# Kernel optimization log

Hardware: AMD Instinct MI355X
Metric: run time of the kernel (lower is better)

## Reference

```python
import jax, jax.numpy as jnp
import numpy as np

# --- static configuration (from init_kwargs / chosen original_size) ---
IMG = 1024            # PromptGetter image_size
DS = 64               # PromptGetter downsizing
ORIG_H, ORIG_W = 1080, 1920
SCALE = IMG / max(ORIG_H, ORIG_W)                 # ResizeLongestSide scale
PRE_H = int(np.floor(ORIG_H * SCALE + 0.5))       # get_prepadded_size -> 576
PRE_W = int(np.floor(ORIG_W * SCALE + 0.5))       # -> 1024
NW = int(ORIG_W * SCALE) // DS                    # grid columns (n_w)
NUM_GRIDS = (IMG // DS) ** 2                      # safe upper bound on grid ids (256)
DEFAULT_THR_TARGET = 0.65
NUM_BG = 1
NUM_LABELS = 16


def setup_inputs() -> dict:
    key = jax.random.key(0)
    k1, k2 = jax.random.split(key)
    return {
        "image_embeddings": jax.random.normal(k1, (1, 256, 64, 64), dtype=jnp.float32),
        "reference_feats": jax.random.normal(k2, (NUM_LABELS, 1, 256), dtype=jnp.float32),
        "original_size": jnp.array([ORIG_H, ORIG_W], dtype=jnp.int32),
        "threshold": jnp.zeros((1, 1), dtype=jnp.float32),  # 0 -> default_threshold_target
        "num_bg_points": 1,
    }


def _postprocess(sim):
    """SAM postprocess_masks: 64x64 -> IMGxIMG -> crop prepadded -> original size."""
    m = jax.image.resize(sim, (IMG, IMG), method="linear")  # align_corners=False bilinear
    m = m[:PRE_H, :PRE_W]
    return jax.image.resize(m, (ORIG_H, ORIG_W), method="linear")


def _point_selection(mask_sim, thr):
    h, w = mask_sim.shape
    flat = mask_sim.reshape(-1)

    # background: k lowest-similarity points (topk largest=False)
    _, bg_idx = jax.lax.top_k(-flat, NUM_BG)
    bg_row = bg_idx // w
    bg_col = bg_idx - bg_row * w
    bg_coords = jnp.stack([bg_col, bg_row], axis=-1).astype(jnp.float32)  # (NUM_BG, 2) as (x, y)

    # foreground: per-grid-cell best-scoring point above threshold.
    # The original gathers torch.where(mask_sim > thr) points and picks the max
    # score per downsized grid cell; here we keep fixed shapes by masking and
    # doing a segment-max over all pixels (same selected points/scores).
    idx = jnp.arange(h * w)
    ys = idx // w
    xs = idx % w
    valid = flat > thr
    grid = ((jnp.floor(ys * SCALE / DS)) * NW + jnp.floor(xs * SCALE / DS)).astype(jnp.int32)
    score = jnp.where(valid, flat, -jnp.inf)
    best = jax.ops.segment_max(score, grid, num_segments=NUM_GRIDS)
    is_best = valid & (flat == best[grid])
    cand = jnp.where(is_best, idx, h * w)
    best_idx = jax.ops.segment_min(cand, grid, num_segments=NUM_GRIDS)  # first max, like torch.topk(k=1)
    grid_ok = jnp.isfinite(best) & (best_idx < h * w)
    safe_idx = jnp.minimum(best_idx, h * w - 1)
    bx = jnp.where(grid_ok, (safe_idx % w).astype(jnp.float32), 0.0)
    by = jnp.where(grid_ok, (safe_idx // w).astype(jnp.float32), 0.0)
    sc = jnp.where(grid_ok, best, -jnp.inf)
    pts = jnp.stack([bx, by, sc], axis=-1)  # (NUM_GRIDS, 3) = (x, y, score)

    # sort by score, descending (empty grid cells sink to the end with -inf)
    order = jnp.argsort(-pts[:, -1])
    return pts[order], bg_coords


def reference(image_embeddings, reference_feats, original_size, threshold, num_bg_points):
    tf = image_embeddings[0]                                   # (C, H, W)
    tf = tf / jnp.linalg.norm(tf, axis=0, keepdims=True)       # channelwise L2 normalize
    c = tf.shape[0]
    tf = tf.reshape(c, -1)                                     # (C, HW)
    thr = ((threshold == 0).astype(threshold.dtype) * DEFAULT_THR_TARGET + threshold)[0, 0]

    def per_label(ref_feat):                                   # ref_feat (1, C)
        sim = (ref_feat @ tf).reshape(64, 64)                  # cosine sim map
        return _point_selection(_postprocess(sim), thr)

    points_scores, bg_coords = jax.vmap(per_label)(reference_feats)
    return points_scores, bg_coords
```

## Files before the change

kernel.cpp:

```cpp
#include <hip/hip_runtime.h>
#include <cmath>
#include <climits>

#define NLAB 16
#define GRIDS 144
#define HOUT 1080
#define WOUT 1920
#define KS2 0.53333336f
#define KS1 0.0625f
#define NEG_MARK -1.0e30f
#define POS_BIG   1.0e30f

__device__ __forceinline__ void taps64(int i, int& t0, int& t1, float& g) {
    float s = ((float)i + 0.5f) * KS1 - 0.5f;
    float f = floorf(s);
    g = s - f;
    int j = (int)f;
    t0 = j < 0 ? 0 : j;
    t1 = j + 1; if (t1 > 63) t1 = 63;
}

__device__ __forceinline__ void fused_taps(int P, int n1m1, int& base,
                                           float& w0, float& w1, float& w2) {
    float sx = ((float)P + 0.5f) * KS2 - 0.5f;
    float fx = floorf(sx);
    float bx = sx - fx;
    int tx = (int)fx;
    int i0 = tx < 0 ? 0 : tx;
    int i1 = tx + 1; if (i1 > n1m1) i1 = n1m1;
    int a0, a1; float ga; taps64(i0, a0, a1, ga);
    int b0, b1; float gb; taps64(i1, b0, b1, gb);
    base = a0;
    w0 = (1.f - bx) * (1.f - ga); w1 = 0.f; w2 = 0.f;
    float c1 = (1.f - bx) * ga;
    if (a1 == base) w0 += c1; else w1 += c1;
    float c2 = bx * (1.f - gb);
    { int o = b0 - base; if (o == 0) w0 += c2; else if (o == 1) w1 += c2; else w2 += c2; }
    float c3 = bx * gb;
    { int o = b1 - base; if (o == 0) w0 += c3; else if (o == 1) w1 += c3; else w2 += c3; }
}

__launch_bounds__(256)
__global__ void sim_kernel(const float* __restrict__ emb,
                           const float* __restrict__ ref,
                           float* __restrict__ sim) {
    __shared__ float rlds[NLAB * 256];
    __shared__ float red[16][NLAB][16];
    __shared__ float n2red[16][16];
    int tid = threadIdx.x;
    for (int i = tid; i < NLAB * 256; i += 256) rlds[i] = ref[i];
    __syncthreads();
    int posl = tid & 15;
    int chunk = tid >> 4;
    int p = blockIdx.x * 16 + posl;
    float acc[NLAB];
#pragma unroll
    for (int l = 0; l < NLAB; ++l) acc[l] = 0.f;
    float n2 = 0.f;
    int cbase = chunk * 16;
#pragma unroll
    for (int cc = 0; cc < 16; ++cc) {
        int c = cbase + cc;
        float v = emb[c * 4096 + p];
        n2 = fmaf(v, v, n2);
#pragma unroll
        for (int l = 0; l < NLAB; ++l)
            acc[l] = fmaf(rlds[l * 256 + c], v, acc[l]);
    }
#pragma unroll
    for (int l = 0; l < NLAB; ++l) red[posl][l][chunk] = acc[l];
    n2red[posl][chunk] = n2;
    __syncthreads();
    int l = chunk;
    float dot = 0.f, nn = 0.f;
#pragma unroll
    for (int k = 0; k < 16; ++k) { dot += red[posl][l][k]; nn += n2red[posl][k]; }
    sim[l * 4096 + p] = dot / sqrtf(nn);
}

__launch_bounds__(256)
__global__ void eval_kernel(const float* __restrict__ simAll,
                            const float* __restrict__ thrPtr,
                            float* __restrict__ gVal, int* __restrict__ gIdx,
                            float* __restrict__ mVal, int* __restrict__ mIdx) {
    int label = blockIdx.x / GRIDS;
    int g = blockIdx.x - label * GRIDS;
    int gy = g >> 4, gx = g & 15;
    int tid = threadIdx.x;

    __shared__ float s8[8][9];
    __shared__ float4 wxT[120];
    __shared__ float4 wyT[120];
    __shared__ float rv[4], rmv[4];
    __shared__ int   ri[4], rmi[4];

    int X0 = gx * 120, Y0 = gy * 120;
    int r0, c0; float dw0, dw1, dw2;
    fused_taps(Y0, 575, r0, dw0, dw1, dw2);
    fused_taps(X0, 1023, c0, dw0, dw1, dw2);

    if (tid < 64) {
        int j = tid >> 3, k = tid & 7;
        int rr = r0 + j; if (rr > 63) rr = 63;
        int kk = c0 + k; if (kk > 63) kk = 63;
        s8[j][k] = simAll[label * 4096 + rr * 64 + kk];
    }
    if (tid < 120) {
        int kb; float w0, w1, w2;
        fused_taps(X0 + tid, 1023, kb, w0, w1, w2);
        wxT[tid] = make_float4(w0, w1, w2, __int_as_float(kb - c0));
    } else if (tid >= 128 && tid < 248) {
        int r = tid - 128;
        int rb; float w0, w1, w2;
        fused_taps(Y0 + r, 575, rb, w0, w1, w2);
        wyT[r] = make_float4(w0, w1, w2, __int_as_float(rb - r0));
    }
    __syncthreads();

    float t0v = thrPtr[0];
    float thr = (t0v == 0.0f) ? 0.65f : t0v;

    float bmax = NEG_MARK; int bidx = INT_MAX;
    float vmin = POS_BIG;  int vidx = INT_MAX;

    if (tid < 240) {
        int h = (tid >= 120) ? 1 : 0;
        int c = tid - h * 120;
        float4 wx = wxT[c];
        int kb = __float_as_int(wx.w);
        const int ybase = h * 60;
        int idx = (Y0 + ybase) * WOUT + X0 + c;
        int rcur = -1;
        float t0 = 0.f, t1 = 0.f, t2 = 0.f;
#pragma unroll 4
        for (int r = 0; r < 60; ++r) {
            float4 wy = wyT[ybase + r];
            int rb = __float_as_int(wy.w);
            if (rb != rcur) {
                rcur = rb;
                const float* p0 = &s8[rb][kb];
                const float* p1 = &s8[rb + 1][kb];
                const float* p2 = &s8[rb + 2][kb];
                t0 = fmaf(wx.z, p0[2], fmaf(wx.y, p0[1], wx.x * p0[0]));
                t1 = fmaf(wx.z, p1[2], fmaf(wx.y, p1[1], wx.x * p1[0]));
                t2 = fmaf(wx.z, p2[2], fmaf(wx.y, p2[1], wx.x * p2[0]));
            }
            float val = fmaf(wy.z, t2, fmaf(wy.y, t1, wy.x * t0));
            if (val > bmax) { bmax = val; bidx = idx; }
            if (val < vmin) { vmin = val; vidx = idx; }
            idx += WOUT;
        }
    }

    for (int off = 32; off; off >>= 1) {
        float ov = __shfl_xor(bmax, off); int oi = __shfl_xor(bidx, off);
        if (ov > bmax || (ov == bmax && oi < bidx)) { bmax = ov; bidx = oi; }
        float mv2 = __shfl_xor(vmin, off); int mi2 = __shfl_xor(vidx, off);
        if (mv2 < vmin || (mv2 == vmin && mi2 < vidx)) { vmin = mv2; vidx = mi2; }
    }
    int wave = tid >> 6;
    if ((tid & 63) == 0) { rv[wave] = bmax; ri[wave] = bidx; rmv[wave] = vmin; rmi[wave] = vidx; }
    __syncthreads();
    if (tid == 0) {
#pragma unroll
        for (int w = 1; w < 4; ++w) {
            float ov = rv[w]; int oi = ri[w];
            if (ov > rv[0] || (ov == rv[0] && oi < ri[0])) { rv[0] = ov; ri[0] = oi; }
            float mv2 = rmv[w]; int mi2 = rmi[w];
            if (mv2 < rmv[0] || (mv2 == rmv[0] && mi2 < rmi[0])) { rmv[0] = mv2; rmi[0] = mi2; }
        }
        int o = label * GRIDS + g;
        if (rv[0] > thr) { gVal[o] = rv[0]; gIdx[o] = ri[0]; }
        else             { gVal[o] = NEG_MARK; gIdx[o] = INT_MAX; }
        mVal[o] = rmv[0]; mIdx[o] = rmi[0];
    }
}

__launch_bounds__(256)
__global__ void final_kernel(const float* __restrict__ gVal, const int* __restrict__ gIdx,
                             const float* __restrict__ mVal, const int* __restrict__ mIdx,
                             float* __restrict__ out) {
    int l = blockIdx.x;
    int tid = threadIdx.x;
    __shared__ float sc[256]; __shared__ int sg[256];
    __shared__ float lx[256], ly[256];

    float score = NEG_MARK;
    float x = 0.0f, y = 0.0f;
    if (tid < GRIDS) {
        float v = gVal[l * GRIDS + tid];
        int i = gIdx[l * GRIDS + tid];
        if (v != NEG_MARK && i < HOUT * WOUT) {
            score = v;
            x = (float)(i % WOUT);
            y = (float)(i / WOUT);
        }
    }
    sc[tid] = score; sg[tid] = tid; lx[tid] = x; ly[tid] = y;
    __syncthreads();

    for (int k = 2; k <= 256; k <<= 1) {
        for (int j = k >> 1; j > 0; j >>= 1) {
            int i2 = tid ^ j;
            if (i2 > tid) {
                float s_a = sc[tid], s_b = sc[i2];
                int g_a = sg[tid], g_b = sg[i2];
                bool up = ((tid & k) == 0);
                bool b_before_a = (s_b > s_a) || (s_b == s_a && g_b < g_a);
                if (b_before_a == up) {
                    sc[tid] = s_b; sc[i2] = s_a;
                    sg[tid] = g_b; sg[i2] = g_a;
                }
            }
            __syncthreads();
        }
    }

    int g2 = sg[tid];
    float* o = out + (l * 256 + tid) * 3;
    o[0] = lx[g2]; o[1] = ly[g2]; o[2] = sc[tid];

    __shared__ float mv[256]; __shared__ int mi[256];
    float v2 = POS_BIG; int i3 = INT_MAX;
    if (tid < GRIDS) { v2 = mVal[l * GRIDS + tid]; i3 = mIdx[l * GRIDS + tid]; }
    mv[tid] = v2; mi[tid] = i3;
    __syncthreads();
    for (int s2 = 128; s2 > 0; s2 >>= 1) {
        if (tid < s2) {
            float ov = mv[tid + s2]; int oi = mi[tid + s2];
            if (ov < mv[tid] || (ov == mv[tid] && oi < mi[tid])) { mv[tid] = ov; mi[tid] = oi; }
        }
        __syncthreads();
    }
    if (tid == 0) {
        int bi = mi[0];
        out[NLAB * 256 * 3 + l * 2 + 0] = (float)(bi % WOUT);
        out[NLAB * 256 * 3 + l * 2 + 1] = (float)(bi / WOUT);
    }
}

extern "C" void kernel_launch(void* const* d_in, const int* in_sizes, int n_in,
                              void* d_out, int out_size, void* d_ws, size_t ws_size,
                              hipStream_t stream) {
    const float* emb = (const float*)d_in[0];
    const float* ref = (const float*)d_in[1];
    const float* thr = (const float*)d_in[3];
    float* out = (float*)d_out;

    float* sim  = (float*)d_ws;
    float* gVal = sim + NLAB * 4096;
    int*   gIdx = (int*)(gVal + NLAB * GRIDS);
    float* mVal = (float*)(gIdx + NLAB * GRIDS);
    int*   mIdx = (int*)(mVal + NLAB * GRIDS);

    sim_kernel<<<256, 256, 0, stream>>>(emb, ref, sim);
    eval_kernel<<<NLAB * GRIDS, 256, 0, stream>>>(sim, thr, gVal, gIdx, mVal, mIdx);
    final_kernel<<<NLAB, 256, 0, stream>>>(gVal, gIdx, mVal, mIdx, out);
}
```

Before: 90.72 us.

## Fuse cosine-similarity computation into eval kernel, recomputing 8x8 patch per block

Removes the separate sim_kernel and its workspace round-trip. Each eval block now computes the 8x8 patch of cosine similarities it needs straight from the embeddings, with 4 threads per position splitting the 256 channels and reducing via shuffles. This saves one kernel launch and one global write/read pass. In exchange the embedding reads and norms are recomputed redundantly across the 2304 blocks (about 64 positions x 256 channels each), which adds memory traffic, though mostly through cache.

```diff
diff --git a/kernel.cpp b/kernel.cpp
--- a/kernel.cpp
+++ b/kernel.cpp
@@ -41,48 +41,11 @@
 }
 
 __launch_bounds__(256)
-__global__ void sim_kernel(const float* __restrict__ emb,
-                           const float* __restrict__ ref,
-                           float* __restrict__ sim) {
-    __shared__ float rlds[NLAB * 256];
-    __shared__ float red[16][NLAB][16];
-    __shared__ float n2red[16][16];
-    int tid = threadIdx.x;
-    for (int i = tid; i < NLAB * 256; i += 256) rlds[i] = ref[i];
-    __syncthreads();
-    int posl = tid & 15;
-    int chunk = tid >> 4;
-    int p = blockIdx.x * 16 + posl;
-    float acc[NLAB];
-#pragma unroll
-    for (int l = 0; l < NLAB; ++l) acc[l] = 0.f;
-    float n2 = 0.f;
-    int cbase = chunk * 16;
-#pragma unroll
-    for (int cc = 0; cc < 16; ++cc) {
-        int c = cbase + cc;
-        float v = emb[c * 4096 + p];
-        n2 = fmaf(v, v, n2);
-#pragma unroll
-        for (int l = 0; l < NLAB; ++l)
-            acc[l] = fmaf(rlds[l * 256 + c], v, acc[l]);
-    }
-#pragma unroll
-    for (int l = 0; l < NLAB; ++l) red[posl][l][chunk] = acc[l];
-    n2red[posl][chunk] = n2;
-    __syncthreads();
-    int l = chunk;
-    float dot = 0.f, nn = 0.f;
-#pragma unroll
-    for (int k = 0; k < 16; ++k) { dot += red[posl][l][k]; nn += n2red[posl][k]; }
-    sim[l * 4096 + p] = dot / sqrtf(nn);
-}
-
-__launch_bounds__(256)
-__global__ void eval_kernel(const float* __restrict__ simAll,
-                            const float* __restrict__ thrPtr,
-                            float* __restrict__ gVal, int* __restrict__ gIdx,
-                            float* __restrict__ mVal, int* __restrict__ mIdx) {
+__global__ void simeval_kernel(const float* __restrict__ emb,
+                               const float* __restrict__ ref,
+                               const float* __restrict__ thrPtr,
+                               float* __restrict__ gVal, int* __restrict__ gIdx,
+                               float* __restrict__ mVal, int* __restrict__ mIdx) {
     int label = blockIdx.x / GRIDS;
     int g = blockIdx.x - label * GRIDS;
     int gy = g >> 4, gx = g & 15;
@@ -99,12 +62,27 @@
     fused_taps(Y0, 575, r0, dw0, dw1, dw2);
     fused_taps(X0, 1023, c0, dw0, dw1, dw2);
 
-    if (tid < 64) {
-        int j = tid >> 3, k = tid & 7;
+    {
+        int pos = tid >> 2;
+        int q = tid & 3;
+        int j = pos >> 3, k = pos & 7;
         int rr = r0 + j; if (rr > 63) rr = 63;
         int kk = c0 + k; if (kk > 63) kk = 63;
-        s8[j][k] = simAll[label * 4096 + rr * 64 + kk];
-    }
+        int p = rr * 64 + kk;
+        const float* eb = emb + q * 64 * 4096 + p;
+        const float* rf = ref + label * 256 + q * 64;
+        float dot = 0.f, n2 = 0.f;
+#pragma unroll 8
+        for (int cc = 0; cc < 64; ++cc) {
+            float v = eb[cc * 4096];
+            dot = fmaf(rf[cc], v, dot);
+            n2 = fmaf(v, v, n2);
+        }
+        dot += __shfl_xor(dot, 1); dot += __shfl_xor(dot, 2);
+        n2  += __shfl_xor(n2, 1);  n2  += __shfl_xor(n2, 2);
+        if (q == 0) s8[j][k] = dot / sqrtf(n2);
+    }
+
     if (tid < 120) {
         int kb; float w0, w1, w2;
         fused_taps(X0 + tid, 1023, kb, w0, w1, w2);
@@ -247,13 +225,11 @@
     const float* thr = (const float*)d_in[3];
     float* out = (float*)d_out;
 
-    float* sim  = (float*)d_ws;
-    float* gVal = sim + NLAB * 4096;
+    float* gVal = (float*)d_ws;
     int*   gIdx = (int*)(gVal + NLAB * GRIDS);
     float* mVal = (float*)(gIdx + NLAB * GRIDS);
     int*   mIdx = (int*)(mVal + NLAB * GRIDS);
 
-    sim_kernel<<<256, 256, 0, stream>>>(emb, ref, sim);
-    eval_kernel<<<NLAB * GRIDS, 256, 0, stream>>>(sim, thr, gVal, gIdx, mVal, mIdx);
+    simeval_kernel<<<NLAB * GRIDS, 256, 0, stream>>>(emb, ref, thr, gVal, gIdx, mVal, mIdx);
     final_kernel<<<NLAB, 256, 0, stream>>>(gVal, gIdx, mVal, mIdx, out);
 }
```

Result: slower. 115.9 us (+27.7%).
